# Kernel optimization log

Hardware: AMD Instinct MI355X
Metric: run time of the kernel (lower is better)

## Reference

```python
import jax, jax.numpy as jnp
import numpy as np

B, S, D, H, E = 4, 1024, 1024, 16, 4
HD = D // H
EPS = 1e-5


def setup_inputs() -> dict:
    key = jax.random.key(0)
    ks = jax.random.split(key, 6)
    std = 0.02
    return {
        "hidden_states": jax.random.normal(ks[0], (B, S, D), dtype=jnp.float32),
        "Wr": jax.random.normal(ks[1], (D, E), dtype=jnp.float32) * std,
        "br": jnp.zeros((E,), jnp.float32),
        "ln_g": jnp.ones((E, D), jnp.float32),
        "ln_b": jnp.zeros((E, D), jnp.float32),
        "W_attn": jax.random.normal(ks[2], (E, D, 3 * D), dtype=jnp.float32) * std,
        "b_attn": jnp.zeros((E, 3 * D), jnp.float32),
        "W_proj": jax.random.normal(ks[3], (E, D, D), dtype=jnp.float32) * std,
        "b_proj": jnp.zeros((E, D), jnp.float32),
    }


def reference(hidden_states, Wr, br, ln_g, ln_b, W_attn, b_attn, W_proj, b_proj):
    b, s, d = hidden_states.shape
    x = hidden_states.reshape(b * s, d)  # [N, D]

    # naive softmax router over experts
    score = jax.nn.softmax(x @ Wr + br, axis=-1)  # [N, E]

    # LayerNorm stats are expert-independent; affine is per-expert
    mu = jnp.mean(x, axis=-1, keepdims=True)
    var = jnp.mean(jnp.square(x - mu), axis=-1, keepdims=True)
    xn = (x - mu) * jax.lax.rsqrt(var + EPS)  # [N, D]

    ln_out = xn[:, None, :] * ln_g[None] + ln_b[None]  # [N, E, D]
    qkv_all = jnp.einsum('ned,edf->nef', ln_out, W_attn) + b_attn  # [N, E, 3D]
    # weighted_qkv: scale each expert's qkv by its routing score, sum
    qkv = jnp.einsum('ne,nef->nf', score, qkv_all)  # [N, 3D]

    q, k, v = jnp.split(qkv.reshape(b, s, 3 * d), 3, axis=-1)
    def split_heads(t):
        return t.reshape(b, s, H, HD).transpose(0, 2, 1, 3)  # [B,H,S,hd]
    q, k, v = split_heads(q), split_heads(k), split_heads(v)

    scale = 1.0 / jnp.sqrt(jnp.asarray(HD, q.dtype))
    att = jnp.einsum('bhqd,bhkd->bhqk', q, k) * scale  # [B,H,S,S]
    causal = jnp.tril(jnp.ones((s, s), dtype=bool))
    att = jnp.where(causal[None, None], att, jnp.finfo(att.dtype).min)
    probs = jax.nn.softmax(att, axis=-1)
    ctx = jnp.einsum('bhqk,bhkd->bhqd', probs, v)  # [B,H,S,hd]
    ctx = ctx.transpose(0, 2, 1, 3).reshape(b * s, d)  # [N, D]

    proj_all = jnp.einsum('nd,edf->nef', ctx, W_proj) + b_proj  # [N, E, D]
    out = jnp.einsum('ne,nef->nf', score, proj_all).reshape(b, s, d)
    return out
```

## Files before the change

kernel.cpp:

```cpp
#include <hip/hip_runtime.h>
#include <stdint.h>

#define NB 4
#define SS 1024
#define DD 1024
#define EE 4
#define HH 16
#define HDD 64
#define NN (NB*SS)
#define KK2 (EE*DD)
#define FF1 (3*DD)

typedef __attribute__((ext_vector_type(4))) float f32x4;
typedef __attribute__((ext_vector_type(8))) _Float16 half8;
typedef __attribute__((ext_vector_type(4))) _Float16 half4;

static __device__ __forceinline__ f32x4 mfma16(half8 a, half8 b, f32x4 c){
  return __builtin_amdgcn_mfma_f32_16x16x32_f16(a, b, c, 0, 0, 0);
}

#define GLOAD_LDS16(gp, lp) __builtin_amdgcn_global_load_lds( \
    (const unsigned int __attribute__((address_space(1)))*)(uintptr_t)(gp), \
    (unsigned int __attribute__((address_space(3)))*)(uintptr_t)(lp), 16, 0, 0)

#define SBAR() do { asm volatile("" ::: "memory"); \
                    __builtin_amdgcn_s_barrier(); \
                    asm volatile("" ::: "memory"); } while(0)

__global__ __launch_bounds__(256) void prep_kernel(
    const float* __restrict__ x, const float* __restrict__ Wr,
    const float* __restrict__ br, float* __restrict__ score,
    _Float16* __restrict__ xnb)
{
  int n = blockIdx.x;
  int tid = threadIdx.x;
  float4 xv = ((const float4*)(x + (size_t)n*DD))[tid];
  float xa[4] = {xv.x, xv.y, xv.z, xv.w};
  float vals[6];
  vals[0] = xa[0]+xa[1]+xa[2]+xa[3];
  vals[1] = xa[0]*xa[0]+xa[1]*xa[1]+xa[2]*xa[2]+xa[3]*xa[3];
  vals[2] = vals[3] = vals[4] = vals[5] = 0.f;
  #pragma unroll
  for (int j = 0; j < 4; ++j){
    float4 w = ((const float4*)Wr)[tid*4 + j];
    vals[2] += xa[j]*w.x; vals[3] += xa[j]*w.y;
    vals[4] += xa[j]*w.z; vals[5] += xa[j]*w.w;
  }
  #pragma unroll
  for (int off = 32; off >= 1; off >>= 1)
    #pragma unroll
    for (int i = 0; i < 6; ++i)
      vals[i] += __shfl_xor(vals[i], off, 64);
  __shared__ float red[4][6];
  int wid = tid >> 6;
  if ((tid & 63) == 0){
    #pragma unroll
    for (int i = 0; i < 6; ++i) red[wid][i] = vals[i];
  }
  __syncthreads();
  float tot[6];
  #pragma unroll
  for (int i = 0; i < 6; ++i)
    tot[i] = red[0][i] + red[1][i] + red[2][i] + red[3][i];

  float mu   = tot[0] * (1.f/DD);
  float var  = tot[1] * (1.f/DD) - mu*mu;
  float rsig = rsqrtf(var + 1e-5f);
  float lg[4];
  #pragma unroll
  for (int e = 0; e < 4; ++e) lg[e] = tot[2+e] + br[e];
  float mx = fmaxf(fmaxf(lg[0], lg[1]), fmaxf(lg[2], lg[3]));
  float ex[4], esum = 0.f;
  #pragma unroll
  for (int e = 0; e < 4; ++e){ ex[e] = __expf(lg[e] - mx); esum += ex[e]; }
  if (tid < 4) score[n*4 + tid] = ex[tid] / esum;

  half4 o;
  #pragma unroll
  for (int j = 0; j < 4; ++j) o[j] = (_Float16)((xa[j] - mu) * rsig);
  *(half4*)(xnb + (size_t)n*DD + tid*4) = o;
}

template<bool AFFINE>
__global__ __launch_bounds__(256) void transpose_f16_kernel(
    const float* __restrict__ W, _Float16* __restrict__ WT, int K, int F,
    const float* __restrict__ gvec, const float* __restrict__ bvec,
    float* __restrict__ part)
{
  __shared__ float t[64][65];
  __shared__ float red2[16][64];
  int k0 = blockIdx.x * 64, f0 = blockIdx.y * 64;
  int tid = threadIdx.x;
  int r = tid >> 4, c4 = (tid & 15) * 4;
  float pf[4] = {0.f, 0.f, 0.f, 0.f};
  #pragma unroll
  for (int i = 0; i < 4; ++i){
    int k = k0 + i*16 + r;
    float4 v = *(const float4*)(W + (size_t)k*F + f0 + c4);
    if constexpr (AFFINE){
      float bk = bvec[k];
      pf[0] += bk*v.x; pf[1] += bk*v.y; pf[2] += bk*v.z; pf[3] += bk*v.w;
      float gk = gvec[k];
      v.x *= gk; v.y *= gk; v.z *= gk; v.w *= gk;
    }
    t[i*16 + r][c4+0] = v.x; t[i*16 + r][c4+1] = v.y;
    t[i*16 + r][c4+2] = v.z; t[i*16 + r][c4+3] = v.w;
  }
  if constexpr (AFFINE){
    #pragma unroll
    for (int j = 0; j < 4; ++j) red2[r][c4+j] = pf[j];
  }
  __syncthreads();
  int f = tid >> 2, seg = tid & 3;
  half8 o0, o1;
  #pragma unroll
  for (int j = 0; j < 8; ++j){
    o0[j] = (_Float16)t[seg*16 + j][f];
    o1[j] = (_Float16)t[seg*16 + 8 + j][f];
  }
  _Float16* dst = WT + (size_t)(f0 + f)*K + k0 + seg*16;
  *(half8*)dst = o0;
  *(half8*)(dst + 8) = o1;
  if constexpr (AFFINE){
    if (tid < 64){
      float s = 0.f;
      #pragma unroll
      for (int rr = 0; rr < 16; ++rr) s += red2[rr][tid];
      part[(size_t)blockIdx.x * F + f0 + tid] = s;
    }
  }
}

__global__ __launch_bounds__(256) void bb1_kernel(
    const float* __restrict__ b_attn, const float* __restrict__ part,
    float* __restrict__ BB1)
{
  int idx = blockIdx.x*256 + threadIdx.x;
  int e = idx / FF1, f = idx - e*FF1;
  float s = b_attn[idx];
  #pragma unroll
  for (int i = 0; i < 16; ++i)
    s += part[(size_t)(e*16 + i)*FF1 + f];
  BB1[idx] = s;
}

#define G1_BM 256
#define G1_BN 192
#define G1_BK 64
#define G1_T  (KK2/G1_BK)
#define G1_ABUF (G1_BM*G1_BK)
#define G1_BBUF (G1_BN*G1_BK)
#define G1_BUFSZ (G1_ABUF+G1_BBUF)

__global__ __launch_bounds__(512, 2) void gemm1_kernel(
    const _Float16* __restrict__ XN, const _Float16* __restrict__ BT,
    const float* __restrict__ score, const float* __restrict__ bias,
    _Float16* __restrict__ C)
{
  __shared__ _Float16 smem[2*G1_BUFSZ];
  int tid = threadIdx.x;
  int lane = tid & 63, wid = tid >> 6;
  int q = lane & 15, g = lane >> 4;
  int wr = wid >> 1, wc = wid & 1;
  int xo = (q & 7) << 3;
  int bid = blockIdx.x;
  int xcd = bid & 7, li = bid >> 3;
  int m0 = (li >> 1) * G1_BM;
  int n0 = (xcd*2 + (li & 1)) * G1_BN;

  int arow[4], brow[6];
  #pragma unroll
  for (int mf = 0; mf < 4; ++mf) arow[mf] = (wr*64 + mf*16 + q)*64;
  #pragma unroll
  for (int nf = 0; nf < 6; ++nf) brow[nf] = G1_ABUF + (wc*96 + nf*16 + q)*64;
  int soff[2] = { (g*8) ^ xo, (32 + g*8) ^ xo };

  auto stageA = [&](int t, int buf, int h){
    const int d0 = (t & 15) * G1_BK;
    _Float16* sA = smem + buf*G1_BUFSZ;
    #pragma unroll
    for (int ld = 0; ld < 2; ++ld){
      int l = h*2 + ld;
      int c = l*512 + tid;
      int row = c >> 3;
      int seg = (c & 7) ^ (row & 7);
      GLOAD_LDS16(XN + (size_t)(m0 + row)*DD + d0 + seg*8,
                  sA + (l*512 + wid*64)*8);
    }
  };
  auto stageB = [&](int t, int buf){
    const int k0 = t * G1_BK;
    _Float16* sB = smem + buf*G1_BUFSZ + G1_ABUF;
    #pragma unroll
    for (int ld = 0; ld < 3; ++ld){
      int c = ld*512 + tid;
      int row = c >> 3;
      int seg = (c & 7) ^ (row & 7);
      GLOAD_LDS16(BT + (size_t)(n0 + row)*KK2 + k0 + seg*8,
                  sB + (ld*512 + wid*64)*8);
    }
  };

  f32x4 acc[4][6] = {};
  half8 af0[2][2], af2[2][2], bf[6][2];

  stageA(0, 0, 0); stageA(0, 0, 1); stageB(0, 0);

  for (int t = 0; t < G1_T-1; ++t){
    if (t && (t & 15) == 0){
      int e = t >> 4;
      #pragma unroll
      for (int mf = 0; mf < 4; ++mf)
        #pragma unroll
        for (int r = 0; r < 4; ++r){
          int gm = m0 + wr*64 + mf*16 + g*4 + r;
          float2 s2 = *(const float2*)(score + gm*4 + (e-1));
          float ratio = s2.x / s2.y;
          #pragma unroll
          for (int nf = 0; nf < 6; ++nf)
            acc[mf][nf][r] *= ratio;
        }
    }
    int buf = t & 1, nxt = buf ^ 1;
    const _Float16* base = smem + buf*G1_BUFSZ;
    stageA(t+1, nxt, 0);
    asm volatile("s_waitcnt vmcnt(2)" ::: "memory");
    SBAR();
    #pragma unroll
    for (int m = 0; m < 2; ++m)
      #pragma unroll
      for (int k = 0; k < 2; ++k)
        af0[m][k] = *(const half8*)(base + arow[m] + soff[k]);
    #pragma unroll
    for (int n = 0; n < 3; ++n)
      #pragma unroll
      for (int k = 0; k < 2; ++k)
        bf[n][k] = *(const half8*)(base + brow[n] + soff[k]);
    stageA(t+1, nxt, 1);
    __builtin_amdgcn_s_setprio(1);
    #pragma unroll
    for (int k = 0; k < 2; ++k)
      #pragma unroll
      for (int m = 0; m < 2; ++m)
        #pragma unroll
        for (int n = 0; n < 3; ++n)
          acc[m][n] = mfma16(af0[m][k], bf[n][k], acc[m][n]);
    __builtin_amdgcn_s_setprio(0);
    SBAR();
    #pragma unroll
    for (int n = 3; n < 6; ++n)
      #pragma unroll
      for (int k = 0; k < 2; ++k)
        bf[n][k] = *(const half8*)(base + brow[n] + soff[k]);
    stageB(t+1, nxt);
    __builtin_amdgcn_s_setprio(1);
    #pragma unroll
    for (int k = 0; k < 2; ++k)
      #pragma unroll
      for (int m = 0; m < 2; ++m)
        #pragma unroll
        for (int n = 3; n < 6; ++n)
          acc[m][n] = mfma16(af0[m][k], bf[n][k], acc[m][n]);
    __builtin_amdgcn_s_setprio(0);
    SBAR();
    #pragma unroll
    for (int m = 0; m < 2; ++m)
      #pragma unroll
      for (int k = 0; k < 2; ++k)
        af2[m][k] = *(const half8*)(base + arow[2+m] + soff[k]);
    __builtin_amdgcn_s_setprio(1);
    #pragma unroll
    for (int k = 0; k < 2; ++k)
      #pragma unroll
      for (int m = 0; m < 2; ++m)
        #pragma unroll
        for (int n = 3; n < 6; ++n)
          acc[2+m][n] = mfma16(af2[m][k], bf[n][k], acc[2+m][n]);
    __builtin_amdgcn_s_setprio(0);
    SBAR();
    __builtin_amdgcn_s_setprio(1);
    #pragma unroll
    for (int k = 0; k < 2; ++k)
      #pragma unroll
      for (int m = 0; m < 2; ++m)
        #pragma unroll
        for (int n = 0; n < 3; ++n)
          acc[2+m][n] = mfma16(af2[m][k], bf[n][k], acc[2+m][n]);
    __builtin_amdgcn_s_setprio(0);
  }
  {
    const _Float16* base = smem + ((G1_T-1) & 1)*G1_BUFSZ;
    asm volatile("s_waitcnt vmcnt(0)" ::: "memory");
    SBAR();
    #pragma unroll
    for (int m = 0; m < 2; ++m)
      #pragma unroll
      for (int k = 0; k < 2; ++k){
        af0[m][k] = *(const half8*)(base + arow[m] + soff[k]);
        af2[m][k] = *(const half8*)(base + arow[2+m] + soff[k]);
      }
    #pragma unroll
    for (int n = 0; n < 6; ++n)
      #pragma unroll
      for (int k = 0; k < 2; ++k)
        bf[n][k] = *(const half8*)(base + brow[n] + soff[k]);
    #pragma unroll
    for (int k = 0; k < 2; ++k)
      #pragma unroll
      for (int m = 0; m < 2; ++m)
        #pragma unroll
        for (int n = 0; n < 6; ++n){
          acc[m][n]   = mfma16(af0[m][k], bf[n][k], acc[m][n]);
          acc[2+m][n] = mfma16(af2[m][k], bf[n][k], acc[2+m][n]);
        }
  }

  float bv[6][4];
  #pragma unroll
  for (int nf = 0; nf < 6; ++nf){
    int gn = n0 + wc*96 + nf*16 + q;
    #pragma unroll
    for (int e = 0; e < 4; ++e) bv[nf][e] = bias[e*FF1 + gn];
  }
  #pragma unroll
  for (int mf = 0; mf < 4; ++mf){
    #pragma unroll
    for (int r = 0; r < 4; ++r){
      int gm = m0 + wr*64 + mf*16 + g*4 + r;
      float4 sc = *(const float4*)(score + gm*4);
      #pragma unroll
      for (int nf = 0; nf < 6; ++nf){
        int gn = n0 + wc*96 + nf*16 + q;
        float v = acc[mf][nf][r]*sc.w
                + sc.x*bv[nf][0] + sc.y*bv[nf][1] + sc.z*bv[nf][2] + sc.w*bv[nf][3];
        C[(size_t)gm*FF1 + gn] = (_Float16)v;
      }
    }
  }
}

#define G2_BK 64
#define G2_ABUF (128*G2_BK)
#define G2_BUFSZ (2*G2_ABUF)

__global__ __launch_bounds__(512) void gemm2_kernel(
    const _Float16* __restrict__ CTX, const _Float16* __restrict__ BT,
    const float* __restrict__ score, const float* __restrict__ bias,
    float* __restrict__ Cout)
{
  __shared__ _Float16 smem[2*G2_BUFSZ];
  int tid = threadIdx.x;
  int lane = tid & 63, wid = tid >> 6;
  int q = lane & 15, g = lane >> 4;
  int wr = wid >> 2, wc = wid & 3;
  int xo = (q & 7) << 3;
  int bid = blockIdx.x;
  int xcd = bid >> 5, idx = bid & 31;
  int m0 = (xcd*4 + (idx >> 3)) * 128;
  int n0 = (idx & 7) * 128;

  int arow[4], brow[2];
  #pragma unroll
  for (int mf = 0; mf < 4; ++mf) arow[mf] = (wr*64 + mf*16 + q)*64;
  #pragma unroll
  for (int nf = 0; nf < 2; ++nf) brow[nf] = G2_ABUF + (wc*32 + nf*16 + q)*64;
  int soff[2] = { (g*8) ^ xo, (32 + g*8) ^ xo };

  auto stage = [&](int t, int buf){
    const int d0 = (t & 15) * G2_BK;
    const int k0 = t * G2_BK;
    _Float16* sA = smem + buf*G2_BUFSZ;
    _Float16* sB = sA + G2_ABUF;
    #pragma unroll
    for (int ld = 0; ld < 2; ++ld){
      int c = ld*512 + tid;
      int row = c >> 3;
      int seg = (c & 7) ^ (row & 7);
      GLOAD_LDS16(CTX + (size_t)(m0 + row)*DD + d0 + seg*8,
                  sA + (ld*512 + wid*64)*8);
    }
    #pragma unroll
    for (int ld = 0; ld < 2; ++ld){
      int c = ld*512 + tid;
      int row = c >> 3;
      int seg = (c & 7) ^ (row & 7);
      GLOAD_LDS16(BT + (size_t)(n0 + row)*KK2 + k0 + seg*8,
                  sB + (ld*512 + wid*64)*8);
    }
  };

  f32x4 accp[4][2] = {}, acco[4][2] = {};

  auto compute = [&](int buf){
    const _Float16* base = smem + buf*G2_BUFSZ;
    half8 af[4][2], bfr[2][2];
    #pragma unroll
    for (int m = 0; m < 4; ++m)
      #pragma unroll
      for (int k = 0; k < 2; ++k)
        af[m][k] = *(const half8*)(base + arow[m] + soff[k]);
    #pragma unroll
    for (int n = 0; n < 2; ++n)
      #pragma unroll
      for (int k = 0; k < 2; ++k)
        bfr[n][k] = *(const half8*)(base + brow[n] + soff[k]);
    __builtin_amdgcn_s_setprio(1);
    #pragma unroll
    for (int k = 0; k < 2; ++k)
      #pragma unroll
      for (int m = 0; m < 4; ++m)
        #pragma unroll
        for (int n = 0; n < 2; ++n)
          accp[m][n] = mfma16(af[m][k], bfr[n][k], accp[m][n]);
    __builtin_amdgcn_s_setprio(0);
  };

  auto merge = [&](int e){
    #pragma unroll
    for (int m = 0; m < 4; ++m)
      #pragma unroll
      for (int r = 0; r < 4; ++r){
        int gm = m0 + wr*64 + m*16 + g*4 + r;
        float s = score[(size_t)gm*4 + e];
        #pragma unroll
        for (int n = 0; n < 2; ++n){
          acco[m][n][r] += s*accp[m][n][r];
          accp[m][n][r] = 0.f;
        }
      }
  };

  stage(0, 0);
  for (int t = 0; t < KK2/G2_BK - 1; ++t){
    stage(t+1, (t+1)&1);
    asm volatile("s_waitcnt vmcnt(4)" ::: "memory");
    SBAR();
    compute(t & 1);
    SBAR();
    if ((t & 15) == 15) merge(t >> 4);
  }
  asm volatile("s_waitcnt vmcnt(0)" ::: "memory");
  SBAR();
  compute((KK2/G2_BK - 1) & 1);
  merge(3);

  #pragma unroll
  for (int m = 0; m < 4; ++m){
    #pragma unroll
    for (int r = 0; r < 4; ++r){
      int gm = m0 + wr*64 + m*16 + g*4 + r;
      float4 sc = *(const float4*)(score + gm*4);
      #pragma unroll
      for (int n = 0; n < 2; ++n){
        int gn = n0 + wc*32 + n*16 + q;
        float v = acco[m][n][r]
                + sc.x*bias[gn] + sc.y*bias[DD+gn]
                + sc.z*bias[2*DD+gn] + sc.w*bias[3*DD+gn];
        Cout[(size_t)gm*DD + gn] = v;
      }
    }
  }
}

__global__ __launch_bounds__(256) void attn_kernel(
    const _Float16* __restrict__ qkv, _Float16* __restrict__ ctx)
{
  __shared__ _Float16 lsK[64*64];
  __shared__ _Float16 lsV[64*64];
  __shared__ _Float16 lsP[4][16*64];
  int bh = blockIdx.x, qt = blockIdx.y;
  int b = bh >> 4, h = bh & 15;
  int tid = threadIdx.x, lane = tid & 63, wid = tid >> 6;
  int q = lane & 15, g = lane >> 4;
  int xo = (q & 7) << 3;
  int qrow0 = qt*64 + wid*16;

  half8 qf[2];
  #pragma unroll
  for (int kk = 0; kk < 2; ++kk)
    qf[kk] = *(const half8*)(qkv + ((size_t)b*SS + qrow0 + q)*FF1 + h*HDD + kk*32 + g*8);

  f32x4 o[4] = {};
  float mrow = -1e30f, lsum = 0.f;
  const float SC2 = 0.18033688011112042f;
  int qglob = qrow0 + q;

  for (int kt = 0; kt <= qt; ++kt){
    __syncthreads();
    size_t kvrow = (size_t)b*SS + kt*64;
    #pragma unroll
    for (int i = 0; i < 2; ++i){
      int c = i*256 + tid;
      int row = c >> 3, seg = (c & 7) ^ (row & 7);
      GLOAD_LDS16(qkv + (kvrow + row)*FF1 + DD + h*HDD + seg*8,
                  lsK + (size_t)(i*256 + wid*64)*8);
    }
    #pragma unroll
    for (int i = 0; i < 2; ++i){
      int p = wid*2 + i;
      half8 v = *(const half8*)(qkv + (kvrow + lane)*FF1 + 2*DD + h*HDD + p*8);
      #pragma unroll
      for (int j = 0; j < 8; ++j){
        int hd = p*8 + j;
        lsV[hd*64 + (lane ^ ((hd & 7) << 3))] = v[j];
      }
    }
    __syncthreads();

    f32x4 st[4] = {};
    #pragma unroll
    for (int i = 0; i < 4; ++i){
      #pragma unroll
      for (int kk = 0; kk < 2; ++kk){
        half8 kf = *(const half8*)(lsK + (i*16 + q)*64 + ((kk*32 + g*8) ^ xo));
        st[i] = mfma16(kf, qf[kk], st[i]);
      }
    }
    float pvv[16]; float tm = -1e30f;
    #pragma unroll
    for (int i = 0; i < 4; ++i)
      #pragma unroll
      for (int r = 0; r < 4; ++r){
        int kglob = kt*64 + i*16 + g*4 + r;
        float sv = (kglob <= qglob) ? st[i][r]*SC2 : -1e30f;
        pvv[i*4+r] = sv; tm = fmaxf(tm, sv);
      }
    tm = fmaxf(tm, __shfl_xor(tm, 16, 64));
    tm = fmaxf(tm, __shfl_xor(tm, 32, 64));
    float mnew  = fmaxf(mrow, tm);
    float alpha = exp2f(mrow - mnew);
    mrow = mnew;
    float psum = 0.f;
    _Float16 pb[16];
    #pragma unroll
    for (int i = 0; i < 16; ++i){
      float p = exp2f(pvv[i] - mnew);
      psum += p; pb[i] = (_Float16)p;
    }
    lsum = lsum*alpha + psum;
    float af4[4];
    #pragma unroll
    for (int r = 0; r < 4; ++r) af4[r] = __shfl(alpha, g*4 + r, 64);
    #pragma unroll
    for (int n = 0; n < 4; ++n)
      #pragma unroll
      for (int r = 0; r < 4; ++r) o[n][r] *= af4[r];
    #pragma unroll
    for (int i = 0; i < 4; ++i){
      half4 w4;
      w4[0]=pb[i*4+0]; w4[1]=pb[i*4+1]; w4[2]=pb[i*4+2]; w4[3]=pb[i*4+3];
      *(half4*)(&lsP[wid][q*64 + ((i*16 + g*4) ^ xo)]) = w4;
    }
    #pragma unroll
    for (int kk = 0; kk < 2; ++kk){
      half8 pf = *(const half8*)(&lsP[wid][q*64 + ((kk*32 + g*8) ^ xo)]);
      #pragma unroll
      for (int n = 0; n < 4; ++n){
        half8 vf = *(const half8*)(&lsV[(n*16 + q)*64 + ((kk*32 + g*8) ^ xo)]);
        o[n] = mfma16(pf, vf, o[n]);
      }
    }
  }
  float lt = lsum + __shfl_xor(lsum, 16, 64);
  lt = lt + __shfl_xor(lt, 32, 64);
  float rinv = 1.f / lt;
  #pragma unroll
  for (int r = 0; r < 4; ++r){
    float ri = __shfl(rinv, g*4 + r, 64);
    int qg = qt*64 + wid*16 + g*4 + r;
    _Float16* obase = ctx + ((size_t)b*SS + qg)*DD + h*HDD;
    #pragma unroll
    for (int n = 0; n < 4; ++n)
      obase[n*16 + q] = (_Float16)(o[n][r] * ri);
  }
}

extern "C" void kernel_launch(void* const* d_in, const int* in_sizes, int n_in,
                              void* d_out, int out_size, void* d_ws, size_t ws_size,
                              hipStream_t stream)
{
  const float* x      = (const float*)d_in[0];
  const float* Wr     = (const float*)d_in[1];
  const float* br     = (const float*)d_in[2];
  const float* ln_g   = (const float*)d_in[3];
  const float* ln_b   = (const float*)d_in[4];
  const float* W_attn = (const float*)d_in[5];
  const float* b_attn = (const float*)d_in[6];
  const float* W_proj = (const float*)d_in[7];
  const float* b_proj = (const float*)d_in[8];
  (void)in_sizes; (void)n_in; (void)out_size; (void)ws_size;

  char* ws = (char*)d_ws;
  size_t off = 0;
  auto alloc = [&](size_t bytes) -> void* {
    void* p = ws + off; off += (bytes + 255) & ~(size_t)255; return p;
  };
  _Float16* W1gT  = (_Float16*)alloc((size_t)FF1*KK2*2);
  _Float16* W2T   = (_Float16*)alloc((size_t)DD*KK2*2);
  float*    score = (float*)   alloc((size_t)NN*4*4);
  _Float16* xn16  = (_Float16*)alloc((size_t)NN*DD*2);
  _Float16* qkv   = (_Float16*)alloc((size_t)NN*FF1*2);
  _Float16* ctx   = (_Float16*)alloc((size_t)NN*DD*2);
  float*    part  = (float*)   alloc((size_t)(KK2/64)*FF1*4);
  float*    BB1   = (float*)   alloc((size_t)EE*FF1*4);

  hipLaunchKernelGGL((transpose_f16_kernel<true>), dim3(KK2/64, FF1/64), dim3(256), 0, stream,
                     W_attn, W1gT, KK2, FF1, ln_g, ln_b, part);
  hipLaunchKernelGGL((transpose_f16_kernel<false>), dim3(KK2/64, DD/64), dim3(256), 0, stream,
                     W_proj, W2T, KK2, DD, nullptr, nullptr, nullptr);
  hipLaunchKernelGGL(bb1_kernel, dim3(EE*FF1/256), dim3(256), 0, stream,
                     b_attn, part, BB1);
  hipLaunchKernelGGL(prep_kernel, dim3(NN), dim3(256), 0, stream,
                     x, Wr, br, score, xn16);
  hipLaunchKernelGGL(gemm1_kernel, dim3(256), dim3(512), 0, stream,
                     xn16, W1gT, score, BB1, qkv);
  hipLaunchKernelGGL(attn_kernel, dim3(NB*HH, SS/64), dim3(256), 0, stream,
                     qkv, ctx);
  hipLaunchKernelGGL(gemm2_kernel, dim3(256), dim3(512), 0, stream,
                     ctx, W2T, score, b_proj, (float*)d_out);
}
```

Before: 208.7 us.

## Switch GEMM kernels to 32x32x16 MFMA tiles and restage GEMM2 loads

Both expert GEMMs move from 16x16x32 MFMA fragments to 32x32x16 MFMA fragments, so each wave issues fewer MFMA instructions and fewer LDS fragment reads per K-step. The accumulator row mapping, score rescaling and epilogue indexing are rewritten for the 32x32 output layout. GEMM2 also splits its staging into separate A and B loads, issues the next B tile after the current fragment reads, and splits the MFMA work across a barrier, matching GEMM1's pipeline. This risks LDS bank conflicts, since the swizzle now uses lane bits for 32-row fragments, and the larger accumulator fragments add register pressure.

```diff
diff --git a/kernel.cpp b/kernel.cpp
--- a/kernel.cpp
+++ b/kernel.cpp
@@ -12,11 +12,15 @@
 #define FF1 (3*DD)
 
 typedef __attribute__((ext_vector_type(4))) float f32x4;
+typedef __attribute__((ext_vector_type(16))) float f32x16;
 typedef __attribute__((ext_vector_type(8))) _Float16 half8;
 typedef __attribute__((ext_vector_type(4))) _Float16 half4;
 
 static __device__ __forceinline__ f32x4 mfma16(half8 a, half8 b, f32x4 c){
   return __builtin_amdgcn_mfma_f32_16x16x32_f16(a, b, c, 0, 0, 0);
+}
+static __device__ __forceinline__ f32x16 mfma32(half8 a, half8 b, f32x16 c){
+  return __builtin_amdgcn_mfma_f32_32x32x16_f16(a, b, c, 0, 0, 0);
 }
 
 #define GLOAD_LDS16(gp, lp) __builtin_amdgcn_global_load_lds( \
@@ -160,20 +164,22 @@
   __shared__ _Float16 smem[2*G1_BUFSZ];
   int tid = threadIdx.x;
   int lane = tid & 63, wid = tid >> 6;
-  int q = lane & 15, g = lane >> 4;
+  int q2 = lane & 31, g2 = lane >> 5;
   int wr = wid >> 1, wc = wid & 1;
-  int xo = (q & 7) << 3;
+  int xo = (lane & 7) << 3;
   int bid = blockIdx.x;
   int xcd = bid & 7, li = bid >> 3;
   int m0 = (li >> 1) * G1_BM;
   int n0 = (xcd*2 + (li & 1)) * G1_BN;
 
-  int arow[4], brow[6];
-  #pragma unroll
-  for (int mf = 0; mf < 4; ++mf) arow[mf] = (wr*64 + mf*16 + q)*64;
-  #pragma unroll
-  for (int nf = 0; nf < 6; ++nf) brow[nf] = G1_ABUF + (wc*96 + nf*16 + q)*64;
-  int soff[2] = { (g*8) ^ xo, (32 + g*8) ^ xo };
+  int arow[2], brow[3];
+  #pragma unroll
+  for (int mf = 0; mf < 2; ++mf) arow[mf] = (wr*64 + mf*32 + q2)*64;
+  #pragma unroll
+  for (int nf = 0; nf < 3; ++nf) brow[nf] = G1_ABUF + (wc*96 + nf*32 + q2)*64;
+  int koff[4];
+  #pragma unroll
+  for (int kk = 0; kk < 4; ++kk) koff[kk] = (kk*16 + g2*8) ^ xo;
 
   auto stageA = [&](int t, int buf, int h){
     const int d0 = (t & 15) * G1_BK;
@@ -201,8 +207,8 @@
     }
   };
 
-  f32x4 acc[4][6] = {};
-  half8 af0[2][2], af2[2][2], bf[6][2];
+  f32x16 acc[2][3] = {};
+  half8 af0[4], af1[4], bf[3][4];
 
   stageA(0, 0, 0); stageA(0, 0, 1); stageB(0, 0);
 
@@ -210,15 +216,16 @@
     if (t && (t & 15) == 0){
       int e = t >> 4;
       #pragma unroll
-      for (int mf = 0; mf < 4; ++mf)
+      for (int mf = 0; mf < 2; ++mf)
         #pragma unroll
-        for (int r = 0; r < 4; ++r){
-          int gm = m0 + wr*64 + mf*16 + g*4 + r;
+        for (int reg = 0; reg < 16; ++reg){
+          int row32 = (reg & 3) + 8*(reg >> 2) + 4*g2;
+          int gm = m0 + wr*64 + mf*32 + row32;
           float2 s2 = *(const float2*)(score + gm*4 + (e-1));
           float ratio = s2.x / s2.y;
-          #pragma unroll
-          for (int nf = 0; nf < 6; ++nf)
-            acc[mf][nf][r] *= ratio;
+          acc[mf][0][reg] *= ratio;
+          acc[mf][1][reg] *= ratio;
+          acc[mf][2][reg] *= ratio;
         }
     }
     int buf = t & 1, nxt = buf ^ 1;
@@ -227,65 +234,40 @@
     asm volatile("s_waitcnt vmcnt(2)" ::: "memory");
     SBAR();
     #pragma unroll
-    for (int m = 0; m < 2; ++m)
-      #pragma unroll
-      for (int k = 0; k < 2; ++k)
-        af0[m][k] = *(const half8*)(base + arow[m] + soff[k]);
-    #pragma unroll
-    for (int n = 0; n < 3; ++n)
-      #pragma unroll
-      for (int k = 0; k < 2; ++k)
-        bf[n][k] = *(const half8*)(base + brow[n] + soff[k]);
+    for (int kk = 0; kk < 4; ++kk){
+      af0[kk]  = *(const half8*)(base + arow[0] + koff[kk]);
+      bf[0][kk] = *(const half8*)(base + brow[0] + koff[kk]);
+      bf[1][kk] = *(const half8*)(base + brow[1] + koff[kk]);
+    }
     stageA(t+1, nxt, 1);
     __builtin_amdgcn_s_setprio(1);
     #pragma unroll
-    for (int k = 0; k < 2; ++k)
-      #pragma unroll
-      for (int m = 0; m < 2; ++m)
-        #pragma unroll
-        for (int n = 0; n < 3; ++n)
-          acc[m][n] = mfma16(af0[m][k], bf[n][k], acc[m][n]);
+    for (int kk = 0; kk < 4; ++kk){
+      acc[0][0] = mfma32(af0[kk], bf[0][kk], acc[0][0]);
+      acc[0][1] = mfma32(af0[kk], bf[1][kk], acc[0][1]);
+    }
     __builtin_amdgcn_s_setprio(0);
     SBAR();
     #pragma unroll
-    for (int n = 3; n < 6; ++n)
-      #pragma unroll
-      for (int k = 0; k < 2; ++k)
-        bf[n][k] = *(const half8*)(base + brow[n] + soff[k]);
+    for (int kk = 0; kk < 4; ++kk){
+      bf[2][kk] = *(const half8*)(base + brow[2] + koff[kk]);
+      af1[kk]   = *(const half8*)(base + arow[1] + koff[kk]);
+    }
     stageB(t+1, nxt);
     __builtin_amdgcn_s_setprio(1);
     #pragma unroll
-    for (int k = 0; k < 2; ++k)
-      #pragma unroll
-      for (int m = 0; m < 2; ++m)
-        #pragma unroll
-        for (int n = 3; n < 6; ++n)
-          acc[m][n] = mfma16(af0[m][k], bf[n][k], acc[m][n]);
-    __builtin_amdgcn_s_setprio(0);
-    SBAR();
-    #pragma unroll
-    for (int m = 0; m < 2; ++m)
-      #pragma unroll
-      for (int k = 0; k < 2; ++k)
-        af2[m][k] = *(const half8*)(base + arow[2+m] + soff[k]);
-    __builtin_amdgcn_s_setprio(1);
-    #pragma unroll
-    for (int k = 0; k < 2; ++k)
-      #pragma unroll
-      for (int m = 0; m < 2; ++m)
-        #pragma unroll
-        for (int n = 3; n < 6; ++n)
-          acc[2+m][n] = mfma16(af2[m][k], bf[n][k], acc[2+m][n]);
+    for (int kk = 0; kk < 4; ++kk){
+      acc[0][2] = mfma32(af0[kk], bf[2][kk], acc[0][2]);
+      acc[1][0] = mfma32(af1[kk], bf[0][kk], acc[1][0]);
+    }
     __builtin_amdgcn_s_setprio(0);
     SBAR();
     __builtin_amdgcn_s_setprio(1);
     #pragma unroll
-    for (int k = 0; k < 2; ++k)
-      #pragma unroll
-      for (int m = 0; m < 2; ++m)
-        #pragma unroll
-        for (int n = 0; n < 3; ++n)
-          acc[2+m][n] = mfma16(af2[m][k], bf[n][k], acc[2+m][n]);
+    for (int kk = 0; kk < 4; ++kk){
+      acc[1][1] = mfma32(af1[kk], bf[1][kk], acc[1][1]);
+      acc[1][2] = mfma32(af1[kk], bf[2][kk], acc[1][2]);
+    }
     __builtin_amdgcn_s_setprio(0);
   }
   {
@@ -293,45 +275,40 @@
     asm volatile("s_waitcnt vmcnt(0)" ::: "memory");
     SBAR();
     #pragma unroll
-    for (int m = 0; m < 2; ++m)
-      #pragma unroll
-      for (int k = 0; k < 2; ++k){
-        af0[m][k] = *(const half8*)(base + arow[m] + soff[k]);
-        af2[m][k] = *(const half8*)(base + arow[2+m] + soff[k]);
+    for (int kk = 0; kk < 4; ++kk){
+      af0[kk] = *(const half8*)(base + arow[0] + koff[kk]);
+      af1[kk] = *(const half8*)(base + arow[1] + koff[kk]);
+      #pragma unroll
+      for (int nf = 0; nf < 3; ++nf)
+        bf[nf][kk] = *(const half8*)(base + brow[nf] + koff[kk]);
+    }
+    #pragma unroll
+    for (int kk = 0; kk < 4; ++kk)
+      #pragma unroll
+      for (int nf = 0; nf < 3; ++nf){
+        acc[0][nf] = mfma32(af0[kk], bf[nf][kk], acc[0][nf]);
+        acc[1][nf] = mfma32(af1[kk], bf[nf][kk], acc[1][nf]);
       }
-    #pragma unroll
-    for (int n = 0; n < 6; ++n)
-      #pragma unroll
-      for (int k = 0; k < 2; ++k)
-        bf[n][k] = *(const half8*)(base + brow[n] + soff[k]);
-    #pragma unroll
-    for (int k = 0; k < 2; ++k)
-      #pragma unroll
-      for (int m = 0; m < 2; ++m)
-        #pragma unroll
-        for (int n = 0; n < 6; ++n){
-          acc[m][n]   = mfma16(af0[m][k], bf[n][k], acc[m][n]);
-          acc[2+m][n] = mfma16(af2[m][k], bf[n][k], acc[2+m][n]);
-        }
-  }
-
-  float bv[6][4];
-  #pragma unroll
-  for (int nf = 0; nf < 6; ++nf){
-    int gn = n0 + wc*96 + nf*16 + q;
+  }
+
+  float bv[3][4];
+  #pragma unroll
+  for (int nf = 0; nf < 3; ++nf){
+    int gn = n0 + wc*96 + nf*32 + q2;
     #pragma unroll
     for (int e = 0; e < 4; ++e) bv[nf][e] = bias[e*FF1 + gn];
   }
   #pragma unroll
-  for (int mf = 0; mf < 4; ++mf){
-    #pragma unroll
-    for (int r = 0; r < 4; ++r){
-      int gm = m0 + wr*64 + mf*16 + g*4 + r;
+  for (int mf = 0; mf < 2; ++mf){
+    #pragma unroll
+    for (int reg = 0; reg < 16; ++reg){
+      int row32 = (reg & 3) + 8*(reg >> 2) + 4*g2;
+      int gm = m0 + wr*64 + mf*32 + row32;
       float4 sc = *(const float4*)(score + gm*4);
       #pragma unroll
-      for (int nf = 0; nf < 6; ++nf){
-        int gn = n0 + wc*96 + nf*16 + q;
-        float v = acc[mf][nf][r]*sc.w
+      for (int nf = 0; nf < 3; ++nf){
+        int gn = n0 + wc*96 + nf*32 + q2;
+        float v = acc[mf][nf][reg]*sc.w
                 + sc.x*bv[nf][0] + sc.y*bv[nf][1] + sc.z*bv[nf][2] + sc.w*bv[nf][3];
         C[(size_t)gm*FF1 + gn] = (_Float16)v;
       }
@@ -351,26 +328,25 @@
   __shared__ _Float16 smem[2*G2_BUFSZ];
   int tid = threadIdx.x;
   int lane = tid & 63, wid = tid >> 6;
-  int q = lane & 15, g = lane >> 4;
+  int q2 = lane & 31, g2 = lane >> 5;
   int wr = wid >> 2, wc = wid & 3;
-  int xo = (q & 7) << 3;
+  int xo = (lane & 7) << 3;
   int bid = blockIdx.x;
   int xcd = bid >> 5, idx = bid & 31;
   int m0 = (xcd*4 + (idx >> 3)) * 128;
   int n0 = (idx & 7) * 128;
 
-  int arow[4], brow[2];
-  #pragma unroll
-  for (int mf = 0; mf < 4; ++mf) arow[mf] = (wr*64 + mf*16 + q)*64;
-  #pragma unroll
-  for (int nf = 0; nf < 2; ++nf) brow[nf] = G2_ABUF + (wc*32 + nf*16 + q)*64;
-  int soff[2] = { (g*8) ^ xo, (32 + g*8) ^ xo };
-
-  auto stage = [&](int t, int buf){
+  int arow[2], brow;
+  #pragma unroll
+  for (int mf = 0; mf < 2; ++mf) arow[mf] = (wr*64 + mf*32 + q2)*64;
+  brow = G2_ABUF + (wc*32 + q2)*64;
+  int koff[4];
+  #pragma unroll
+  for (int kk = 0; kk < 4; ++kk) koff[kk] = (kk*16 + g2*8) ^ xo;
+
+  auto stageA = [&](int t, int buf){
     const int d0 = (t & 15) * G2_BK;
-    const int k0 = t * G2_BK;
     _Float16* sA = smem + buf*G2_BUFSZ;
-    _Float16* sB = sA + G2_ABUF;
     #pragma unroll
     for (int ld = 0; ld < 2; ++ld){
       int c = ld*512 + tid;
@@ -379,6 +355,10 @@
       GLOAD_LDS16(CTX + (size_t)(m0 + row)*DD + d0 + seg*8,
                   sA + (ld*512 + wid*64)*8);
     }
+  };
+  auto stageB = [&](int t, int buf){
+    const int k0 = t * G2_BK;
+    _Float16* sB = smem + buf*G2_BUFSZ + G2_ABUF;
     #pragma unroll
     for (int ld = 0; ld < 2; ++ld){
       int c = ld*512 + tid;
@@ -389,75 +369,84 @@
     }
   };
 
-  f32x4 accp[4][2] = {}, acco[4][2] = {};
-
-  auto compute = [&](int buf){
-    const _Float16* base = smem + buf*G2_BUFSZ;
-    half8 af[4][2], bfr[2][2];
-    #pragma unroll
-    for (int m = 0; m < 4; ++m)
-      #pragma unroll
-      for (int k = 0; k < 2; ++k)
-        af[m][k] = *(const half8*)(base + arow[m] + soff[k]);
-    #pragma unroll
-    for (int n = 0; n < 2; ++n)
-      #pragma unroll
-      for (int k = 0; k < 2; ++k)
-        bfr[n][k] = *(const half8*)(base + brow[n] + soff[k]);
-    __builtin_amdgcn_s_setprio(1);
-    #pragma unroll
-    for (int k = 0; k < 2; ++k)
-      #pragma unroll
-      for (int m = 0; m < 4; ++m)
-        #pragma unroll
-        for (int n = 0; n < 2; ++n)
-          accp[m][n] = mfma16(af[m][k], bfr[n][k], accp[m][n]);
-    __builtin_amdgcn_s_setprio(0);
-  };
+  f32x16 accp[2] = {}, acco[2] = {};
 
   auto merge = [&](int e){
     #pragma unroll
-    for (int m = 0; m < 4; ++m)
-      #pragma unroll
-      for (int r = 0; r < 4; ++r){
-        int gm = m0 + wr*64 + m*16 + g*4 + r;
+    for (int m = 0; m < 2; ++m)
+      #pragma unroll
+      for (int reg = 0; reg < 16; ++reg){
+        int row32 = (reg & 3) + 8*(reg >> 2) + 4*g2;
+        int gm = m0 + wr*64 + m*32 + row32;
         float s = score[(size_t)gm*4 + e];
-        #pragma unroll
-        for (int n = 0; n < 2; ++n){
-          acco[m][n][r] += s*accp[m][n][r];
-          accp[m][n][r] = 0.f;
-        }
+        acco[m][reg] += s*accp[m][reg];
+        accp[m][reg] = 0.f;
       }
   };
 
-  stage(0, 0);
+  stageA(0, 0); stageB(0, 0);
   for (int t = 0; t < KK2/G2_BK - 1; ++t){
-    stage(t+1, (t+1)&1);
-    asm volatile("s_waitcnt vmcnt(4)" ::: "memory");
+    int buf = t & 1, nxt = buf ^ 1;
+    const _Float16* base = smem + buf*G2_BUFSZ;
+    stageA(t+1, nxt);
+    asm volatile("s_waitcnt vmcnt(2)" ::: "memory");
     SBAR();
-    compute(t & 1);
+    half8 af[2][4], bfr[4];
+    #pragma unroll
+    for (int kk = 0; kk < 4; ++kk){
+      af[0][kk] = *(const half8*)(base + arow[0] + koff[kk]);
+      af[1][kk] = *(const half8*)(base + arow[1] + koff[kk]);
+      bfr[kk]   = *(const half8*)(base + brow + koff[kk]);
+    }
+    stageB(t+1, nxt);
+    __builtin_amdgcn_s_setprio(1);
+    #pragma unroll
+    for (int kk = 0; kk < 2; ++kk){
+      accp[0] = mfma32(af[0][kk], bfr[kk], accp[0]);
+      accp[1] = mfma32(af[1][kk], bfr[kk], accp[1]);
+    }
+    __builtin_amdgcn_s_setprio(0);
     SBAR();
+    __builtin_amdgcn_s_setprio(1);
+    #pragma unroll
+    for (int kk = 2; kk < 4; ++kk){
+      accp[0] = mfma32(af[0][kk], bfr[kk], accp[0]);
+      accp[1] = mfma32(af[1][kk], bfr[kk], accp[1]);
+    }
+    __builtin_amdgcn_s_setprio(0);
     if ((t & 15) == 15) merge(t >> 4);
   }
-  asm volatile("s_waitcnt vmcnt(0)" ::: "memory");
-  SBAR();
-  compute((KK2/G2_BK - 1) & 1);
-  merge(3);
-
-  #pragma unroll
-  for (int m = 0; m < 4; ++m){
-    #pragma unroll
-    for (int r = 0; r < 4; ++r){
-      int gm = m0 + wr*64 + m*16 + g*4 + r;
+  {
+    const _Float16* base = smem + ((KK2/G2_BK - 1) & 1)*G2_BUFSZ;
+    asm volatile("s_waitcnt vmcnt(0)" ::: "memory");
+    SBAR();
+    half8 af[2][4], bfr[4];
+    #pragma unroll
+    for (int kk = 0; kk < 4; ++kk){
+      af[0][kk] = *(const half8*)(base + arow[0] + koff[kk]);
+      af[1][kk] = *(const half8*)(base + arow[1] + koff[kk]);
+      bfr[kk]   = *(const half8*)(base + brow + koff[kk]);
+    }
+    #pragma unroll
+    for (int kk = 0; kk < 4; ++kk){
+      accp[0] = mfma32(af[0][kk], bfr[kk], accp[0]);
+      accp[1] = mfma32(af[1][kk], bfr[kk], accp[1]);
+    }
+    merge(3);
+  }
+
+  #pragma unroll
+  for (int m = 0; m < 2; ++m){
+    #pragma unroll
+    for (int reg = 0; reg < 16; ++reg){
+      int row32 = (reg & 3) + 8*(reg >> 2) + 4*g2;
+      int gm = m0 + wr*64 + m*32 + row32;
       float4 sc = *(const float4*)(score + gm*4);
-      #pragma unroll
-      for (int n = 0; n < 2; ++n){
-        int gn = n0 + wc*32 + n*16 + q;
-        float v = acco[m][n][r]
-                + sc.x*bias[gn] + sc.y*bias[DD+gn]
-                + sc.z*bias[2*DD+gn] + sc.w*bias[3*DD+gn];
-        Cout[(size_t)gm*DD + gn] = v;
-      }
+      int gn = n0 + wc*32 + q2;
+      float v = acco[m][reg]
+              + sc.x*bias[gn] + sc.y*bias[DD+gn]
+              + sc.z*bias[2*DD+gn] + sc.w*bias[3*DD+gn];
+      Cout[(size_t)gm*DD + gn] = v;
     }
   }
 }
```

Result: slower. 232.7 us (+11.5%).

## Double-buffer K/V tiles in attention and precompute expert score ratios

Applied to the files above, without the earlier changes.

The attention kernel now double-buffers K and V in LDS. It prefetches the next tile's K through global_load_lds and V into registers while computing on the current tile, and uses one waitcnt plus barrier pair in place of two syncthreads per iteration. The aim is to hide global load latency behind the QK and PV MFMAs. Separately, prep_kernel now precomputes per-row expert score ratios, so gemm1 loads one float instead of doing a float2 load and a divide at each expert boundary. This costs extra LDS, which can lower occupancy, adds more complex vmcnt accounting, and adds a small extra buffer.

```diff
diff --git a/kernel.cpp b/kernel.cpp
--- a/kernel.cpp
+++ b/kernel.cpp
@@ -30,7 +30,7 @@
 __global__ __launch_bounds__(256) void prep_kernel(
     const float* __restrict__ x, const float* __restrict__ Wr,
     const float* __restrict__ br, float* __restrict__ score,
-    _Float16* __restrict__ xnb)
+    float* __restrict__ ratios, _Float16* __restrict__ xnb)
 {
   int n = blockIdx.x;
   int tid = threadIdx.x;
@@ -73,7 +73,10 @@
   float ex[4], esum = 0.f;
   #pragma unroll
   for (int e = 0; e < 4; ++e){ ex[e] = __expf(lg[e] - mx); esum += ex[e]; }
-  if (tid < 4) score[n*4 + tid] = ex[tid] / esum;
+  if (tid < 4){
+    score[n*4 + tid] = ex[tid] / esum;
+    ratios[n*4 + tid] = (tid > 0) ? (ex[tid-1] / ex[tid]) : 0.f;
+  }
 
   half4 o;
   #pragma unroll
@@ -154,8 +157,8 @@
 
 __global__ __launch_bounds__(512, 2) void gemm1_kernel(
     const _Float16* __restrict__ XN, const _Float16* __restrict__ BT,
-    const float* __restrict__ score, const float* __restrict__ bias,
-    _Float16* __restrict__ C)
+    const float* __restrict__ score, const float* __restrict__ ratios,
+    const float* __restrict__ bias, _Float16* __restrict__ C)
 {
   __shared__ _Float16 smem[2*G1_BUFSZ];
   int tid = threadIdx.x;
@@ -214,8 +217,7 @@
         #pragma unroll
         for (int r = 0; r < 4; ++r){
           int gm = m0 + wr*64 + mf*16 + g*4 + r;
-          float2 s2 = *(const float2*)(score + gm*4 + (e-1));
-          float ratio = s2.x / s2.y;
+          float ratio = ratios[gm*4 + e];
           #pragma unroll
           for (int nf = 0; nf < 6; ++nf)
             acc[mf][nf][r] *= ratio;
@@ -465,8 +467,8 @@
 __global__ __launch_bounds__(256) void attn_kernel(
     const _Float16* __restrict__ qkv, _Float16* __restrict__ ctx)
 {
-  __shared__ _Float16 lsK[64*64];
-  __shared__ _Float16 lsV[64*64];
+  __shared__ _Float16 lsK[2][64*64];
+  __shared__ _Float16 lsV[2][64*64];
   __shared__ _Float16 lsP[4][16*64];
   int bh = blockIdx.x, qt = blockIdx.y;
   int b = bh >> 4, h = bh & 15;
@@ -480,42 +482,62 @@
   for (int kk = 0; kk < 2; ++kk)
     qf[kk] = *(const half8*)(qkv + ((size_t)b*SS + qrow0 + q)*FF1 + h*HDD + kk*32 + g*8);
 
+  auto issueK = [&](int kt, int buf){
+    size_t kvrow = (size_t)b*SS + kt*64;
+    #pragma unroll
+    for (int i = 0; i < 2; ++i){
+      int c = i*256 + tid;
+      int row = c >> 3, seg = (c & 7) ^ (row & 7);
+      GLOAD_LDS16(qkv + (kvrow + row)*FF1 + DD + h*HDD + seg*8,
+                  lsK[buf] + (size_t)(i*256 + wid*64)*8);
+    }
+  };
+  auto issueV = [&](int kt, half8* vr){
+    size_t kvrow = (size_t)b*SS + kt*64;
+    #pragma unroll
+    for (int i = 0; i < 2; ++i)
+      vr[i] = *(const half8*)(qkv + (kvrow + lane)*FF1 + 2*DD + h*HDD + (wid*2+i)*8);
+  };
+  auto writeV = [&](const half8* vr, int buf){
+    #pragma unroll
+    for (int i = 0; i < 2; ++i){
+      int p = wid*2 + i;
+      #pragma unroll
+      for (int j = 0; j < 8; ++j){
+        int hd = p*8 + j;
+        lsV[buf][hd*64 + (lane ^ ((hd & 7) << 3))] = vr[i][j];
+      }
+    }
+  };
+
   f32x4 o[4] = {};
   float mrow = -1e30f, lsum = 0.f;
   const float SC2 = 0.18033688011112042f;
   int qglob = qrow0 + q;
 
+  half8 vr[2];
+  issueK(0, 0);
+  issueV(0, vr);
+
   for (int kt = 0; kt <= qt; ++kt){
-    __syncthreads();
-    size_t kvrow = (size_t)b*SS + kt*64;
-    #pragma unroll
-    for (int i = 0; i < 2; ++i){
-      int c = i*256 + tid;
-      int row = c >> 3, seg = (c & 7) ^ (row & 7);
-      GLOAD_LDS16(qkv + (kvrow + row)*FF1 + DD + h*HDD + seg*8,
-                  lsK + (size_t)(i*256 + wid*64)*8);
-    }
-    #pragma unroll
-    for (int i = 0; i < 2; ++i){
-      int p = wid*2 + i;
-      half8 v = *(const half8*)(qkv + (kvrow + lane)*FF1 + 2*DD + h*HDD + p*8);
-      #pragma unroll
-      for (int j = 0; j < 8; ++j){
-        int hd = p*8 + j;
-        lsV[hd*64 + (lane ^ ((hd & 7) << 3))] = v[j];
-      }
-    }
-    __syncthreads();
+    int cur = kt & 1, nxt = cur ^ 1;
+    int tn = (kt < qt) ? kt+1 : qt;
+    asm volatile("s_waitcnt vmcnt(2)" ::: "memory");
+    SBAR();
 
     f32x4 st[4] = {};
     #pragma unroll
     for (int i = 0; i < 4; ++i){
       #pragma unroll
       for (int kk = 0; kk < 2; ++kk){
-        half8 kf = *(const half8*)(lsK + (i*16 + q)*64 + ((kk*32 + g*8) ^ xo));
+        half8 kf = *(const half8*)(lsK[cur] + (i*16 + q)*64 + ((kk*32 + g*8) ^ xo));
         st[i] = mfma16(kf, qf[kk], st[i]);
       }
     }
+    issueK(tn, nxt);
+    asm volatile("s_waitcnt vmcnt(2)" ::: "memory");
+    writeV(vr, cur);
+
     float pvv[16]; float tm = -1e30f;
     #pragma unroll
     for (int i = 0; i < 4; ++i)
@@ -545,6 +567,11 @@
     for (int n = 0; n < 4; ++n)
       #pragma unroll
       for (int r = 0; r < 4; ++r) o[n][r] *= af4[r];
+    issueV(tn, vr);
+
+    asm volatile("s_waitcnt lgkmcnt(0)" ::: "memory");
+    SBAR();
+
     #pragma unroll
     for (int i = 0; i < 4; ++i){
       half4 w4;
@@ -556,7 +583,7 @@
       half8 pf = *(const half8*)(&lsP[wid][q*64 + ((kk*32 + g*8) ^ xo)]);
       #pragma unroll
       for (int n = 0; n < 4; ++n){
-        half8 vf = *(const half8*)(&lsV[(n*16 + q)*64 + ((kk*32 + g*8) ^ xo)]);
+        half8 vf = *(const half8*)(&lsV[cur][(n*16 + q)*64 + ((kk*32 + g*8) ^ xo)]);
         o[n] = mfma16(pf, vf, o[n]);
       }
     }
@@ -598,6 +625,7 @@
   _Float16* W1gT  = (_Float16*)alloc((size_t)FF1*KK2*2);
   _Float16* W2T   = (_Float16*)alloc((size_t)DD*KK2*2);
   float*    score = (float*)   alloc((size_t)NN*4*4);
+  float*    ratio = (float*)   alloc((size_t)NN*4*4);
   _Float16* xn16  = (_Float16*)alloc((size_t)NN*DD*2);
   _Float16* qkv   = (_Float16*)alloc((size_t)NN*FF1*2);
   _Float16* ctx   = (_Float16*)alloc((size_t)NN*DD*2);
@@ -611,9 +639,9 @@
   hipLaunchKernelGGL(bb1_kernel, dim3(EE*FF1/256), dim3(256), 0, stream,
                      b_attn, part, BB1);
   hipLaunchKernelGGL(prep_kernel, dim3(NN), dim3(256), 0, stream,
-                     x, Wr, br, score, xn16);
+                     x, Wr, br, score, ratio, xn16);
   hipLaunchKernelGGL(gemm1_kernel, dim3(256), dim3(512), 0, stream,
-                     xn16, W1gT, score, BB1, qkv);
+                     xn16, W1gT, score, ratio, BB1, qkv);
   hipLaunchKernelGGL(attn_kernel, dim3(NB*HH, SS/64), dim3(256), 0, stream,
                      qkv, ctx);
   hipLaunchKernelGGL(gemm2_kernel, dim3(256), dim3(512), 0, stream,
```

After: 206.8 us. No clear change (-0.9%).
